# Kernel tuning notes

Measured on AMD Instinct MI355X. Metric: run time of the kernel, lower is better.

The kernel has to match this reference:

```python
import jax, jax.numpy as jnp
import numpy as np

ALPHA = 0.5
EPS = 1e-10

def setup_inputs() -> dict:
    key = jax.random.key(0)
    k1, k2, k3, k4 = jax.random.split(key, 4)
    B, S, H = 8, 2048, 768
    query_embs = jax.random.normal(k1, (B, S, H), dtype=jnp.float32)
    key_embs = jax.random.normal(k2, (B, S, H), dtype=jnp.float32)
    q_mask = (jax.random.uniform(k3, (B, S)) > 0.1).astype(jnp.float32)
    k_mask = (jax.random.uniform(k4, (B, S)) > 0.1).astype(jnp.float32)
    q_mask = q_mask.at[:, 0].set(1.0)
    k_mask = k_mask.at[:, 0].set(1.0)
    return {"query_embs": query_embs, "key_embs": key_embs,
            "q_mask": q_mask, "k_mask": k_mask, "gumbel_temp": 1.0}

def _l2norm(x):
    # torch F.normalize: x / max(||x||, eps-ish); use rsqrt with tiny floor
    n = jnp.sqrt(jnp.sum(x * x, axis=-1, keepdims=True))
    return x / jnp.maximum(n, 1e-12)

def reference(query_embs, key_embs, q_mask, k_mask, gumbel_temp):
    B, S, H = query_embs.shape
    q = _l2norm(query_embs)
    k = _l2norm(key_embs)
    sim = jnp.einsum('bqh,bkh->bqk', q, k)  # [B,S,S]
    # exponential distance decay w_{ij} = exp(-alpha*|i-j|)
    pos = jnp.arange(S)
    dist = jnp.abs(pos[:, None] - pos[None, :]).astype(sim.dtype)
    sim = sim * jnp.exp(-ALPHA * dist)
    valid = q_mask[:, :, None] * k_mask[:, None, :]  # [B,S,S]
    # eval path: no Gumbel noise
    noisy = sim / gumbel_temp
    noisy = noisy * valid - (1.0 - valid) * 1e9
    p = jax.nn.softmax(noisy, axis=-1)
    agg = jnp.einsum('bqk,bkh->bqh', p, k)
    scores = jnp.sum(q * agg, axis=-1) * q_mask  # [B,S]
    denom = jnp.maximum(jnp.sum(q_mask, axis=-1), 1.0)
    return jnp.sum(scores, axis=-1) / denom  # [B]
```

## Files before the change

kernel.cpp:

```cpp
#include <hip/hip_runtime.h>
#include <math.h>

#define SB 8
#define SS 2048
#define SH 768
#define ALPHA 0.5f

typedef __fp16 f16x8 __attribute__((ext_vector_type(8)));
typedef float f32x4 __attribute__((ext_vector_type(4)));

__device__ __forceinline__ float dot4(float4 a, float4 b) {
  return a.x*b.x + a.y*b.y + a.z*b.z + a.w*b.w;
}
__device__ __forceinline__ unsigned int pk2(float a, float b) {
  return __builtin_bit_cast(unsigned int, __builtin_amdgcn_cvt_pkrtz(a, b));
}


__global__ __launch_bounds__(256) void kprep_kernel(
    const float* __restrict__ K, const float* __restrict__ km,
    const float* __restrict__ qm,
    __fp16* __restrict__ Khs, float* __restrict__ ksum,
    float* __restrict__ Nk, float* __restrict__ qsum) {
  __shared__ float4 red[4][3][64];
  int b = blockIdx.y, jc = blockIdx.x, t = threadIdx.x;
  int w = t >> 6, lane = t & 63;
  int j0 = jc * 32;
  float4 acc0 = {0,0,0,0}, acc1 = {0,0,0,0}, acc2 = {0,0,0,0};
  for (int jj = 0; jj < 8; ++jj) {
    int j = j0 + 8 * w + jj;
    const float4* rp = (const float4*)(K + ((size_t)b * SS + j) * SH);
    float4 a = rp[lane], b4 = rp[lane + 64], c4 = rp[lane + 128];
    float ssv = dot4(a, a) + dot4(b4, b4) + dot4(c4, c4);
    #pragma unroll
    for (int m = 1; m < 64; m <<= 1) ssv += __shfl_xor(ssv, m, 64);
    float kwj = km[b * SS + j] / fmaxf(sqrtf(ssv), 1e-12f);
    uint2* kr = (uint2*)(Khs + ((size_t)b * SS + j) * SH);
    kr[lane]       = make_uint2(pk2(a.x*kwj,  a.y*kwj),  pk2(a.z*kwj,  a.w*kwj));
    kr[lane + 64]  = make_uint2(pk2(b4.x*kwj, b4.y*kwj), pk2(b4.z*kwj, b4.w*kwj));
    kr[lane + 128] = make_uint2(pk2(c4.x*kwj, c4.y*kwj), pk2(c4.z*kwj, c4.w*kwj));
    acc0.x += a.x*kwj;  acc0.y += a.y*kwj;  acc0.z += a.z*kwj;  acc0.w += a.w*kwj;
    acc1.x += b4.x*kwj; acc1.y += b4.y*kwj; acc1.z += b4.z*kwj; acc1.w += b4.w*kwj;
    acc2.x += c4.x*kwj; acc2.y += c4.y*kwj; acc2.z += c4.z*kwj; acc2.w += c4.w*kwj;
  }
  red[w][0][lane] = acc0; red[w][1][lane] = acc1; red[w][2][lane] = acc2;
  __syncthreads();
  if (t < 192) {
    int s = t >> 6, l = t & 63;
    float4 r0 = red[0][s][l], r1 = red[1][s][l], r2 = red[2][s][l], r3 = red[3][s][l];
    float* kp = ksum + b * SH + (s * 64 + l) * 4;
    atomicAdd(kp + 0, r0.x+r1.x+r2.x+r3.x);
    atomicAdd(kp + 1, r0.y+r1.y+r2.y+r3.y);
    atomicAdd(kp + 2, r0.z+r1.z+r2.z+r3.z);
    atomicAdd(kp + 3, r0.w+r1.w+r2.w+r3.w);
  }
  if (t < 32) {
    float pkm = km[b * SS + j0 + t];
    float pqm = qm[b * SS + j0 + t];
    #pragma unroll
    for (int m = 1; m < 32; m <<= 1) {
      pkm += __shfl_xor(pkm, m, 64);
      pqm += __shfl_xor(pqm, m, 64);
    }
    if (t == 0) { atomicAdd(&Nk[b], pkm); atomicAdd(&qsum[b], pqm); }
  }
}

__global__ __launch_bounds__(256, 1) void band_kernel(
    const float* __restrict__ Q, const __fp16* __restrict__ Khs,
    const float* __restrict__ temp, const float* __restrict__ qm,
    const float* __restrict__ ksum, const float* __restrict__ Nkp,
    const float* __restrict__ qsum,
    float* __restrict__ acc, int* __restrict__ cnt, float* __restrict__ out) {
  __shared__ float tab_s[64];
  int tid = threadIdx.x;
  int w = tid >> 6, lane = tid & 63;
  int l15 = lane & 15, quad = lane >> 4;
  int blk = blockIdx.x;
  int work = (blk & 7) * 32 + (blk >> 3);
  int b = work >> 5;
  int i0 = (work & 31) * 64;
  int i0w = i0 + 16 * w;
  int qrow = i0w + l15;

  float qmv = qm[b * SS + qrow];
  float nk = Nkp[b];
  {
    float invt = 1.0f / temp[0];
    tab_s[lane] = __expf(-ALPHA * fabsf((float)(lane - 31))) * invt;
  }
  asm volatile("s_waitcnt lgkmcnt(0)" ::: "memory");

  const float* qp = Q + ((size_t)b * SS + qrow) * SH + quad * 8;
  const float* kp = ksum + (size_t)b * SH + quad * 8;
  f16x8 afr[24];
  float ss = 0.f, dd = 0.f;
  #pragma unroll
  for (int s = 0; s < 24; ++s) {
    float4 x0 = *(const float4*)(qp + 32 * s);
    float4 x1 = *(const float4*)(qp + 32 * s + 4);
    float4 k0 = *(const float4*)(kp + 32 * s);
    float4 k1 = *(const float4*)(kp + 32 * s + 4);
    ss += dot4(x0, x0) + dot4(x1, x1);
    dd += dot4(x0, k0) + dot4(x1, k1);
    uint4 u = make_uint4(pk2(x0.x, x0.y), pk2(x0.z, x0.w),
                         pk2(x1.x, x1.y), pk2(x1.z, x1.w));
    afr[s] = __builtin_bit_cast(f16x8, u);
  }
  ss += __shfl_xor(ss, 16, 64); ss += __shfl_xor(ss, 32, 64);
  dd += __shfl_xor(dd, 16, 64); dd += __shfl_xor(dd, 32, 64);
  float qw = qmv / fmaxf(sqrtf(ss), 1e-12f);
  float qwsr[4], d0r[4];
  #pragma unroll
  for (int r = 0; r < 4; ++r) {
    qwsr[r] = __shfl(qw, quad * 4 + r, 64);
    d0r[r]  = __shfl(dd, quad * 4 + r, 64);
  }

  const __fp16* KbH = Khs + (size_t)b * SS * SH;
  f16x8 bqA[12], bqB[12];
  {
    int j = i0w - 32 + l15;
    int jc = min(max(j, 0), SS - 1);
    const __fp16* rp = KbH + (size_t)jc * SH + quad * 8;
    #pragma unroll
    for (int u = 0; u < 12; ++u) bqA[u] = *(const f16x8*)(rp + u * 32);
  }
  float an[4] = {0,0,0,0}, ad[4] = {0,0,0,0};
  f32x4 da = {0,0,0,0}, db = {0,0,0,0};
  #pragma unroll
  for (int fi = 0; fi < 10; ++fi) {
    const int t = fi >> 1, g = fi & 1;
    if (fi < 9) {
      const int tn = (fi + 1) >> 1, gn = (fi + 1) & 1;
      int j = i0w - 32 + 16 * tn + l15;
      int jc = min(max(j, 0), SS - 1);
      const __fp16* rp = KbH + (size_t)jc * SH + gn * 384 + quad * 8;
      #pragma unroll
      for (int u = 0; u < 12; ++u) {
        f16x8 v = *(const f16x8*)(rp + u * 32);
        if (fi & 1) bqA[u] = v; else bqB[u] = v;
      }
    }
    #pragma unroll
    for (int u = 0; u < 12; ++u) {
      f16x8 bv = (fi & 1) ? bqB[u] : bqA[u];
      if (u & 1) db = __builtin_amdgcn_mfma_f32_16x16x32_f16(afr[g*12+u], bv, db, 0, 0, 0);
      else       da = __builtin_amdgcn_mfma_f32_16x16x32_f16(afr[g*12+u], bv, da, 0, 0, 0);
    }
    if (g) {
      f32x4 ds = da + db;
      int j = i0w - 32 + 16 * t + l15;
      float vmask = ((unsigned)j < SS) ? 1.0f : 0.0f;
      int idxb = j - i0w + 31;
      #pragma unroll
      for (int reg = 0; reg < 4; ++reg) {
        float sv = ds[reg] * qwsr[reg];
        int idx = min(max(idxb - quad * 4 - reg, 0), 63);
        float ev = (__expf(sv * tab_s[idx]) - 1.0f) * vmask;
        an[reg] += ev * sv;
        ad[reg] += ev;
      }
      da = (f32x4){0,0,0,0}; db = (f32x4){0,0,0,0};
    }
  }

  float tot = 0.f;
  #pragma unroll
  for (int reg = 0; reg < 4; ++reg) {
    float a = an[reg], e = ad[reg];
    a += __shfl_xor(a, 1, 64); a += __shfl_xor(a, 2, 64);
    a += __shfl_xor(a, 4, 64); a += __shfl_xor(a, 8, 64);
    e += __shfl_xor(e, 1, 64); e += __shfl_xor(e, 2, 64);
    e += __shfl_xor(e, 4, 64); e += __shfl_xor(e, 8, 64);
    tot += (qwsr[reg] * d0r[reg] + a) / (nk + e);
  }
  tot += __shfl_xor(tot, 16, 64);
  tot += __shfl_xor(tot, 32, 64);
  if (lane == 0) {
    atomicAdd(&acc[b], tot);
    __threadfence();
    if (atomicAdd(&cnt[b], 1) == 127) {
      float a2 = atomicAdd(&acc[b], 0.0f);
      out[b] = a2 / fmaxf(qsum[b], 1.0f);
    }
  }
}

extern "C" void kernel_launch(void* const* d_in, const int* in_sizes, int n_in,
                              void* d_out, int out_size, void* d_ws, size_t ws_size,
                              hipStream_t stream) {
  const float* Q    = (const float*)d_in[0];
  const float* K    = (const float*)d_in[1];
  const float* qm   = (const float*)d_in[2];
  const float* km   = (const float*)d_in[3];
  const float* temp = (const float*)d_in[4];
  float* outp = (float*)d_out;

  const size_t KHS_BYTES = (size_t)SB * SS * SH * 2;
  __fp16* Khs = (__fp16*)d_ws;
  float* ksum = (float*)((char*)d_ws + KHS_BYTES);
  float* Nk   = ksum + SB * SH;
  float* qsum = Nk + 8;
  float* accb = qsum + 8;
  int*   cnt  = (int*)(accb + 8);

  (void)hipMemsetAsync(ksum, 0, (SB * SH + 32) * sizeof(float), stream);

  kprep_kernel<<<dim3(64, SB), 256, 0, stream>>>(K, km, qm, Khs, ksum, Nk, qsum);
  band_kernel<<<SB * (SS / 64), 256, 0, stream>>>(Q, Khs, temp, qm, ksum, Nk,
                                                  qsum, accb, cnt, outp);
}
```

Measured before the change: 179.2 us.

## Split band key tiles across wave pairs with explicit asm load pipelining

Each group of 16 query rows is now handled by two waves: one covers key tiles 0-2, the other tiles 3-4. Blocks cover 32 rows instead of 64, the grid doubles to 512 blocks, and launch bounds allow two blocks per CU. This aims to raise occupancy and cut each wave's serial chain of key loads and MFMAs. Key-tile loads are issued with inline global_load asm and explicit vmcnt waits, so loads overlap the MFMAs. Partial sums are combined through LDS before the per-batch atomic. The cost is that both waves of a pair load and normalise the same query rows, and the tile split between the two waves is uneven (three tiles against two).

```diff
diff --git a/kernel.cpp b/kernel.cpp
--- a/kernel.cpp
+++ b/kernel.cpp
@@ -14,6 +14,31 @@
 }
 __device__ __forceinline__ unsigned int pk2(float a, float b) {
   return __builtin_bit_cast(unsigned int, __builtin_amdgcn_cvt_pkrtz(a, b));
+}
+
+#define GLOAD(d, p, imm) \
+  asm volatile("global_load_dwordx4 %0, %1, off offset:" #imm \
+               : "=v"(d) : "v"(p) : "memory")
+#define ISSUE_LO(B, P) do { \
+  GLOAD(B[0],P,0);    GLOAD(B[1],P,64);   GLOAD(B[2],P,128);  \
+  GLOAD(B[3],P,192);  GLOAD(B[4],P,256);  GLOAD(B[5],P,320);  \
+  GLOAD(B[6],P,384);  GLOAD(B[7],P,448);  GLOAD(B[8],P,512);  \
+  GLOAD(B[9],P,576);  GLOAD(B[10],P,640); GLOAD(B[11],P,704); } while (0)
+#define ISSUE_HI(B, P) do { \
+  GLOAD(B[0],P,768);  GLOAD(B[1],P,832);  GLOAD(B[2],P,896);  \
+  GLOAD(B[3],P,960);  GLOAD(B[4],P,1024); GLOAD(B[5],P,1088); \
+  GLOAD(B[6],P,1152); GLOAD(B[7],P,1216); GLOAD(B[8],P,1280); \
+  GLOAD(B[9],P,1344); GLOAD(B[10],P,1408); GLOAD(B[11],P,1472); } while (0)
+#define WAITV(n) asm volatile("s_waitcnt vmcnt(" #n ")" ::: "memory")
+#define SB0() __builtin_amdgcn_sched_barrier(0)
+
+__device__ __forceinline__ void mfma12(const f16x8* a, const f16x8* B,
+                                       f32x4& da, f32x4& db) {
+  #pragma unroll
+  for (int u = 0; u < 12; ++u) {
+    if (u & 1) db = __builtin_amdgcn_mfma_f32_16x16x32_f16(a[u], B[u], db, 0, 0, 0);
+    else       da = __builtin_amdgcn_mfma_f32_16x16x32_f16(a[u], B[u], da, 0, 0, 0);
+  }
 }
 
 
@@ -66,22 +91,26 @@
   }
 }
 
-__global__ __launch_bounds__(256, 1) void band_kernel(
+__global__ __launch_bounds__(256, 2) void band_kernel(
     const float* __restrict__ Q, const __fp16* __restrict__ Khs,
     const float* __restrict__ temp, const float* __restrict__ qm,
     const float* __restrict__ ksum, const float* __restrict__ Nkp,
     const float* __restrict__ qsum,
     float* __restrict__ acc, int* __restrict__ cnt, float* __restrict__ out) {
   __shared__ float tab_s[64];
+  __shared__ float anS[2][2][16], adS[2][2][16];
+  __shared__ float qwS[2][16], d0S[2][16];
   int tid = threadIdx.x;
   int w = tid >> 6, lane = tid & 63;
   int l15 = lane & 15, quad = lane >> 4;
+  int rg = w >> 1, h = w & 1;
   int blk = blockIdx.x;
-  int work = (blk & 7) * 32 + (blk >> 3);
-  int b = work >> 5;
-  int i0 = (work & 31) * 64;
-  int i0w = i0 + 16 * w;
+  int work = (blk & 7) * 64 + (blk >> 3);
+  int b = work >> 6;
+  int i0 = (work & 63) * 32;
+  int i0w = i0 + 16 * rg;
   int qrow = i0w + l15;
+  int jbase = i0w - 32;
 
   float qmv = qm[b * SS + qrow];
   float nk = Nkp[b];
@@ -118,54 +147,55 @@
   }
 
   const __fp16* KbH = Khs + (size_t)b * SS * SH;
-  f16x8 bqA[12], bqB[12];
-  {
-    int j = i0w - 32 + l15;
-    int jc = min(max(j, 0), SS - 1);
-    const __fp16* rp = KbH + (size_t)jc * SH + quad * 8;
-    #pragma unroll
-    for (int u = 0; u < 12; ++u) bqA[u] = *(const f16x8*)(rp + u * 32);
-  }
+  auto tp = [&](int t) {
+    int jc = min(max(jbase + 16 * t + l15, 0), SS - 1);
+    return KbH + (size_t)jc * SH + quad * 8;
+  };
+
   float an[4] = {0,0,0,0}, ad[4] = {0,0,0,0};
   f32x4 da = {0,0,0,0}, db = {0,0,0,0};
-  #pragma unroll
-  for (int fi = 0; fi < 10; ++fi) {
-    const int t = fi >> 1, g = fi & 1;
-    if (fi < 9) {
-      const int tn = (fi + 1) >> 1, gn = (fi + 1) & 1;
-      int j = i0w - 32 + 16 * tn + l15;
-      int jc = min(max(j, 0), SS - 1);
-      const __fp16* rp = KbH + (size_t)jc * SH + gn * 384 + quad * 8;
-      #pragma unroll
-      for (int u = 0; u < 12; ++u) {
-        f16x8 v = *(const f16x8*)(rp + u * 32);
-        if (fi & 1) bqA[u] = v; else bqB[u] = v;
-      }
+  auto epi = [&](int t) {
+    f32x4 ds = da + db;
+    int j = jbase + 16 * t + l15;
+    float vmask = ((unsigned)j < SS) ? 1.0f : 0.0f;
+    int idxb = 16 * t + l15 - 1;
+    #pragma unroll
+    for (int reg = 0; reg < 4; ++reg) {
+      float sv = ds[reg] * qwsr[reg];
+      int idx = min(max(idxb - quad * 4 - reg, 0), 63);
+      float ev = (__expf(sv * tab_s[idx]) - 1.0f) * vmask;
+      an[reg] += ev * sv;
+      ad[reg] += ev;
     }
-    #pragma unroll
-    for (int u = 0; u < 12; ++u) {
-      f16x8 bv = (fi & 1) ? bqB[u] : bqA[u];
-      if (u & 1) db = __builtin_amdgcn_mfma_f32_16x16x32_f16(afr[g*12+u], bv, db, 0, 0, 0);
-      else       da = __builtin_amdgcn_mfma_f32_16x16x32_f16(afr[g*12+u], bv, da, 0, 0, 0);
-    }
-    if (g) {
-      f32x4 ds = da + db;
-      int j = i0w - 32 + 16 * t + l15;
-      float vmask = ((unsigned)j < SS) ? 1.0f : 0.0f;
-      int idxb = j - i0w + 31;
-      #pragma unroll
-      for (int reg = 0; reg < 4; ++reg) {
-        float sv = ds[reg] * qwsr[reg];
-        int idx = min(max(idxb - quad * 4 - reg, 0), 63);
-        float ev = (__expf(sv * tab_s[idx]) - 1.0f) * vmask;
-        an[reg] += ev * sv;
-        ad[reg] += ev;
-      }
-      da = (f32x4){0,0,0,0}; db = (f32x4){0,0,0,0};
-    }
-  }
-
-  float tot = 0.f;
+    da = (f32x4){0,0,0,0}; db = (f32x4){0,0,0,0};
+  };
+
+  f16x8 bqA[12], bqB[12];
+  WAITV(0);
+  if (h == 0) {
+    const __fp16* P0 = tp(0); const __fp16* P1 = tp(1); const __fp16* P2 = tp(2);
+    ISSUE_LO(bqA, P0); ISSUE_HI(bqB, P0);
+    WAITV(12); SB0(); mfma12(afr,      bqA, da, db);
+    ISSUE_LO(bqA, P1);
+    WAITV(12); SB0(); mfma12(afr + 12, bqB, da, db); epi(0);
+    ISSUE_HI(bqB, P1);
+    WAITV(12); SB0(); mfma12(afr,      bqA, da, db);
+    ISSUE_LO(bqA, P2);
+    WAITV(12); SB0(); mfma12(afr + 12, bqB, da, db); epi(1);
+    ISSUE_HI(bqB, P2);
+    WAITV(12); SB0(); mfma12(afr,      bqA, da, db);
+    WAITV(0);  SB0(); mfma12(afr + 12, bqB, da, db); epi(2);
+  } else {
+    const __fp16* P3 = tp(3); const __fp16* P4 = tp(4);
+    ISSUE_LO(bqA, P3); ISSUE_HI(bqB, P3);
+    WAITV(12); SB0(); mfma12(afr,      bqA, da, db);
+    ISSUE_LO(bqA, P4);
+    WAITV(12); SB0(); mfma12(afr + 12, bqB, da, db); epi(3);
+    ISSUE_HI(bqB, P4);
+    WAITV(12); SB0(); mfma12(afr,      bqA, da, db);
+    WAITV(0);  SB0(); mfma12(afr + 12, bqB, da, db); epi(4);
+  }
+
   #pragma unroll
   for (int reg = 0; reg < 4; ++reg) {
     float a = an[reg], e = ad[reg];
@@ -173,16 +203,25 @@
     a += __shfl_xor(a, 4, 64); a += __shfl_xor(a, 8, 64);
     e += __shfl_xor(e, 1, 64); e += __shfl_xor(e, 2, 64);
     e += __shfl_xor(e, 4, 64); e += __shfl_xor(e, 8, 64);
-    tot += (qwsr[reg] * d0r[reg] + a) / (nk + e);
-  }
-  tot += __shfl_xor(tot, 16, 64);
-  tot += __shfl_xor(tot, 32, 64);
-  if (lane == 0) {
-    atomicAdd(&acc[b], tot);
-    __threadfence();
-    if (atomicAdd(&cnt[b], 1) == 127) {
-      float a2 = atomicAdd(&acc[b], 0.0f);
-      out[b] = a2 / fmaxf(qsum[b], 1.0f);
+    if (l15 == 0) { anS[rg][h][quad * 4 + reg] = a; adS[rg][h][quad * 4 + reg] = e; }
+  }
+  if (h == 0 && lane < 16) { qwS[rg][lane] = qw; d0S[rg][lane] = dd; }
+  __syncthreads();
+  if (tid < 32) {
+    int rgc = tid >> 4, rr = tid & 15;
+    float a = anS[rgc][0][rr] + anS[rgc][1][rr];
+    float e = adS[rgc][0][rr] + adS[rgc][1][rr];
+    float sc = (qwS[rgc][rr] * d0S[rgc][rr] + a) / (nk + e);
+    sc += __shfl_xor(sc, 1, 64); sc += __shfl_xor(sc, 2, 64);
+    sc += __shfl_xor(sc, 4, 64); sc += __shfl_xor(sc, 8, 64);
+    sc += __shfl_xor(sc, 16, 64);
+    if (tid == 0) {
+      atomicAdd(&acc[b], sc);
+      __threadfence();
+      if (atomicAdd(&cnt[b], 1) == 63) {
+        float a2 = atomicAdd(&acc[b], 0.0f);
+        out[b] = a2 / fmaxf(qsum[b], 1.0f);
+      }
     }
   }
 }
@@ -208,6 +247,6 @@
   (void)hipMemsetAsync(ksum, 0, (SB * SH + 32) * sizeof(float), stream);
 
   kprep_kernel<<<dim3(64, SB), 256, 0, stream>>>(K, km, qm, Khs, ksum, Nk, qsum);
-  band_kernel<<<SB * (SS / 64), 256, 0, stream>>>(Q, Khs, temp, qm, ksum, Nk,
-                                                  qsum, accb, cnt, outp);
-}
+  band_kernel<<<512, 256, 0, stream>>>(Q, Khs, temp, qm, ksum, Nk,
+                                       qsum, accb, cnt, outp);
+}
```

After: 169.6 us. -5.4%, faster.

## Split hidden dim across waves and raise block count in both kernels

Applied to the files above, without the earlier changes.

The band kernel now gives each block 16 query rows instead of 64. Its four waves each take a 192-wide slice of the hidden dimension, and the partial MFMA tiles plus the norm and dot sums are combined through shared memory before the exp/softmax step. Loads for Q and for the fp16 K tiles are issued with inline global_load_dwordx4, double-buffered and bounded by explicit vmcnt waits, and launch bounds allow 4 blocks per CU. kprep is also re-gridded to 1024 blocks of 16 rows, so both kernels expose more parallel work to hide memory latency. In exchange the kernel pays for an LDS reduction, a __syncthreads, and redundant epilogue work across waves.

```diff
diff --git a/kernel.cpp b/kernel.cpp
--- a/kernel.cpp
+++ b/kernel.cpp
@@ -15,6 +15,15 @@
 __device__ __forceinline__ unsigned int pk2(float a, float b) {
   return __builtin_bit_cast(unsigned int, __builtin_amdgcn_cvt_pkrtz(a, b));
 }
+
+#define GLD(d, p, imm) \
+  asm volatile("global_load_dwordx4 %0, %1, off offset:" #imm \
+               : "=v"(d) : "v"(p) : "memory")
+#define WAITV(n) asm volatile("s_waitcnt vmcnt(" #n ")" ::: "memory")
+#define SB0() __builtin_amdgcn_sched_barrier(0)
+#define ISSUE_B(B, P) do { \
+  GLD(B[0],P,0);   GLD(B[1],P,64);  GLD(B[2],P,128); \
+  GLD(B[3],P,192); GLD(B[4],P,256); GLD(B[5],P,320); } while (0)
 
 
 __global__ __launch_bounds__(256) void kprep_kernel(
@@ -23,12 +32,14 @@
     __fp16* __restrict__ Khs, float* __restrict__ ksum,
     float* __restrict__ Nk, float* __restrict__ qsum) {
   __shared__ float4 red[4][3][64];
-  int b = blockIdx.y, jc = blockIdx.x, t = threadIdx.x;
+  int blk = blockIdx.x, t = threadIdx.x;
   int w = t >> 6, lane = t & 63;
-  int j0 = jc * 32;
+  int work = (blk & 7) * 128 + (blk >> 3);
+  int b = work >> 7;
+  int j0 = (work & 127) * 16;
   float4 acc0 = {0,0,0,0}, acc1 = {0,0,0,0}, acc2 = {0,0,0,0};
-  for (int jj = 0; jj < 8; ++jj) {
-    int j = j0 + 8 * w + jj;
+  for (int jj = 0; jj < 4; ++jj) {
+    int j = j0 + 4 * w + jj;
     const float4* rp = (const float4*)(K + ((size_t)b * SS + j) * SH);
     float4 a = rp[lane], b4 = rp[lane + 64], c4 = rp[lane + 128];
     float ssv = dot4(a, a) + dot4(b4, b4) + dot4(c4, c4);
@@ -54,11 +65,11 @@
     atomicAdd(kp + 2, r0.z+r1.z+r2.z+r3.z);
     atomicAdd(kp + 3, r0.w+r1.w+r2.w+r3.w);
   }
-  if (t < 32) {
+  if (t < 16) {
     float pkm = km[b * SS + j0 + t];
     float pqm = qm[b * SS + j0 + t];
     #pragma unroll
-    for (int m = 1; m < 32; m <<= 1) {
+    for (int m = 1; m < 16; m <<= 1) {
       pkm += __shfl_xor(pkm, m, 64);
       pqm += __shfl_xor(pqm, m, 64);
     }
@@ -66,105 +77,111 @@
   }
 }
 
-__global__ __launch_bounds__(256, 1) void band_kernel(
+__global__ __launch_bounds__(256, 4) void band_kernel(
     const float* __restrict__ Q, const __fp16* __restrict__ Khs,
     const float* __restrict__ temp, const float* __restrict__ qm,
     const float* __restrict__ ksum, const float* __restrict__ Nkp,
     const float* __restrict__ qsum,
     float* __restrict__ acc, int* __restrict__ cnt, float* __restrict__ out) {
+  __shared__ f32x4 sP[4][5][64];
+  __shared__ float sSS[4][16], sDD[4][16];
   __shared__ float tab_s[64];
   int tid = threadIdx.x;
   int w = tid >> 6, lane = tid & 63;
   int l15 = lane & 15, quad = lane >> 4;
   int blk = blockIdx.x;
-  int work = (blk & 7) * 32 + (blk >> 3);
-  int b = work >> 5;
-  int i0 = (work & 31) * 64;
-  int i0w = i0 + 16 * w;
-  int qrow = i0w + l15;
-
-  float qmv = qm[b * SS + qrow];
+  int work = (blk & 7) * 128 + (blk >> 3);
+  int b = work >> 7;
+  int i0 = (work & 127) * 16;
+
+  if (tid < 64) {
+    float invt = 1.0f / temp[0];
+    tab_s[tid] = __expf(-ALPHA * fabsf((float)(tid - 31))) * invt;
+  }
   float nk = Nkp[b];
-  {
-    float invt = 1.0f / temp[0];
-    tab_s[lane] = __expf(-ALPHA * fabsf((float)(lane - 31))) * invt;
-  }
-  asm volatile("s_waitcnt lgkmcnt(0)" ::: "memory");
-
-  const float* qp = Q + ((size_t)b * SS + qrow) * SH + quad * 8;
-  const float* kp = ksum + (size_t)b * SH + quad * 8;
-  f16x8 afr[24];
+
+  const char* qpB = (const char*)(Q + ((size_t)b * SS + i0 + l15) * SH
+                                  + w * 192 + quad * 8);
+  const float* ksb = ksum + (size_t)b * SH + w * 192 + quad * 8;
+  float4 xq[12];
+  GLD(xq[0],qpB,0);    GLD(xq[1],qpB,16);   GLD(xq[2],qpB,128);
+  GLD(xq[3],qpB,144);  GLD(xq[4],qpB,256);  GLD(xq[5],qpB,272);
+  GLD(xq[6],qpB,384);  GLD(xq[7],qpB,400);  GLD(xq[8],qpB,512);
+  GLD(xq[9],qpB,528);  GLD(xq[10],qpB,640); GLD(xq[11],qpB,656);
+  float4 ks0[6], ks1[6];
+  #pragma unroll
+  for (int s = 0; s < 6; ++s) {
+    ks0[s] = *(const float4*)(ksb + 32 * s);
+    ks1[s] = *(const float4*)(ksb + 32 * s + 4);
+  }
+  WAITV(0); SB0();
+  f16x8 afr[6];
   float ss = 0.f, dd = 0.f;
   #pragma unroll
-  for (int s = 0; s < 24; ++s) {
-    float4 x0 = *(const float4*)(qp + 32 * s);
-    float4 x1 = *(const float4*)(qp + 32 * s + 4);
-    float4 k0 = *(const float4*)(kp + 32 * s);
-    float4 k1 = *(const float4*)(kp + 32 * s + 4);
+  for (int s = 0; s < 6; ++s) {
+    float4 x0 = xq[2*s], x1 = xq[2*s+1];
     ss += dot4(x0, x0) + dot4(x1, x1);
-    dd += dot4(x0, k0) + dot4(x1, k1);
+    dd += dot4(x0, ks0[s]) + dot4(x1, ks1[s]);
     uint4 u = make_uint4(pk2(x0.x, x0.y), pk2(x0.z, x0.w),
                          pk2(x1.x, x1.y), pk2(x1.z, x1.w));
     afr[s] = __builtin_bit_cast(f16x8, u);
   }
   ss += __shfl_xor(ss, 16, 64); ss += __shfl_xor(ss, 32, 64);
   dd += __shfl_xor(dd, 16, 64); dd += __shfl_xor(dd, 32, 64);
-  float qw = qmv / fmaxf(sqrtf(ss), 1e-12f);
-  float qwsr[4], d0r[4];
-  #pragma unroll
-  for (int r = 0; r < 4; ++r) {
-    qwsr[r] = __shfl(qw, quad * 4 + r, 64);
-    d0r[r]  = __shfl(dd, quad * 4 + r, 64);
-  }
+  if (quad == 0) { sSS[w][l15] = ss; sDD[w][l15] = dd; }
 
   const __fp16* KbH = Khs + (size_t)b * SS * SH;
-  f16x8 bqA[12], bqB[12];
-  {
-    int j = i0w - 32 + l15;
-    int jc = min(max(j, 0), SS - 1);
-    const __fp16* rp = KbH + (size_t)jc * SH + quad * 8;
+  const char* pt[5];
+  #pragma unroll
+  for (int t = 0; t < 5; ++t) {
+    int jc = min(max(i0 - 32 + 16 * t + l15, 0), SS - 1);
+    pt[t] = (const char*)(KbH + (size_t)jc * SH + w * 192 + quad * 8);
+  }
+  f16x8 bqA[6], bqB[6];
+  auto dotile = [&](f16x8* bq, int t) {
+    f32x4 da = {0,0,0,0}, db = {0,0,0,0};
+    da = __builtin_amdgcn_mfma_f32_16x16x32_f16(afr[0], bq[0], da, 0, 0, 0);
+    db = __builtin_amdgcn_mfma_f32_16x16x32_f16(afr[1], bq[1], db, 0, 0, 0);
+    da = __builtin_amdgcn_mfma_f32_16x16x32_f16(afr[2], bq[2], da, 0, 0, 0);
+    db = __builtin_amdgcn_mfma_f32_16x16x32_f16(afr[3], bq[3], db, 0, 0, 0);
+    da = __builtin_amdgcn_mfma_f32_16x16x32_f16(afr[4], bq[4], da, 0, 0, 0);
+    db = __builtin_amdgcn_mfma_f32_16x16x32_f16(afr[5], bq[5], db, 0, 0, 0);
+    sP[w][t][lane] = da + db;
+  };
+  ISSUE_B(bqA, pt[0]); ISSUE_B(bqB, pt[1]);
+  WAITV(6); SB0(); dotile(bqA, 0); ISSUE_B(bqA, pt[2]);
+  WAITV(6); SB0(); dotile(bqB, 1); ISSUE_B(bqB, pt[3]);
+  WAITV(6); SB0(); dotile(bqA, 2); ISSUE_B(bqA, pt[4]);
+  WAITV(6); SB0(); dotile(bqB, 3);
+  WAITV(0); SB0(); dotile(bqA, 4);
+
+  __syncthreads();
+
+  float qws[4], d0s[4];
+  #pragma unroll
+  for (int reg = 0; reg < 4; ++reg) {
+    int r = quad * 4 + reg;
+    float ssr = sSS[0][r] + sSS[1][r] + sSS[2][r] + sSS[3][r];
+    float ddr = sDD[0][r] + sDD[1][r] + sDD[2][r] + sDD[3][r];
+    qws[reg] = qm[b * SS + i0 + r] / fmaxf(sqrtf(ssr), 1e-12f);
+    d0s[reg] = ddr;
+  }
+  float an[4] = {0,0,0,0}, ad[4] = {0,0,0,0};
+  #pragma unroll
+  for (int t = 0; t < 5; ++t) {
+    f32x4 v = sP[0][t][lane] + sP[1][t][lane] + sP[2][t][lane] + sP[3][t][lane];
+    int j = i0 - 32 + 16 * t + l15;
+    float vmask = ((unsigned)j < SS) ? 1.0f : 0.0f;
+    int idxb = 16 * t + l15 - 1;
     #pragma unroll
-    for (int u = 0; u < 12; ++u) bqA[u] = *(const f16x8*)(rp + u * 32);
-  }
-  float an[4] = {0,0,0,0}, ad[4] = {0,0,0,0};
-  f32x4 da = {0,0,0,0}, db = {0,0,0,0};
-  #pragma unroll
-  for (int fi = 0; fi < 10; ++fi) {
-    const int t = fi >> 1, g = fi & 1;
-    if (fi < 9) {
-      const int tn = (fi + 1) >> 1, gn = (fi + 1) & 1;
-      int j = i0w - 32 + 16 * tn + l15;
-      int jc = min(max(j, 0), SS - 1);
-      const __fp16* rp = KbH + (size_t)jc * SH + gn * 384 + quad * 8;
-      #pragma unroll
-      for (int u = 0; u < 12; ++u) {
-        f16x8 v = *(const f16x8*)(rp + u * 32);
-        if (fi & 1) bqA[u] = v; else bqB[u] = v;
-      }
+    for (int reg = 0; reg < 4; ++reg) {
+      float sv = v[reg] * qws[reg];
+      int idx = min(max(idxb - quad * 4 - reg, 0), 63);
+      float ev = (__expf(sv * tab_s[idx]) - 1.0f) * vmask;
+      an[reg] += ev * sv;
+      ad[reg] += ev;
     }
-    #pragma unroll
-    for (int u = 0; u < 12; ++u) {
-      f16x8 bv = (fi & 1) ? bqB[u] : bqA[u];
-      if (u & 1) db = __builtin_amdgcn_mfma_f32_16x16x32_f16(afr[g*12+u], bv, db, 0, 0, 0);
-      else       da = __builtin_amdgcn_mfma_f32_16x16x32_f16(afr[g*12+u], bv, da, 0, 0, 0);
-    }
-    if (g) {
-      f32x4 ds = da + db;
-      int j = i0w - 32 + 16 * t + l15;
-      float vmask = ((unsigned)j < SS) ? 1.0f : 0.0f;
-      int idxb = j - i0w + 31;
-      #pragma unroll
-      for (int reg = 0; reg < 4; ++reg) {
-        float sv = ds[reg] * qwsr[reg];
-        int idx = min(max(idxb - quad * 4 - reg, 0), 63);
-        float ev = (__expf(sv * tab_s[idx]) - 1.0f) * vmask;
-        an[reg] += ev * sv;
-        ad[reg] += ev;
-      }
-      da = (f32x4){0,0,0,0}; db = (f32x4){0,0,0,0};
-    }
-  }
-
+  }
   float tot = 0.f;
   #pragma unroll
   for (int reg = 0; reg < 4; ++reg) {
@@ -173,11 +190,11 @@
     a += __shfl_xor(a, 4, 64); a += __shfl_xor(a, 8, 64);
     e += __shfl_xor(e, 1, 64); e += __shfl_xor(e, 2, 64);
     e += __shfl_xor(e, 4, 64); e += __shfl_xor(e, 8, 64);
-    tot += (qwsr[reg] * d0r[reg] + a) / (nk + e);
+    tot += (qws[reg] * d0s[reg] + a) / (nk + e);
   }
   tot += __shfl_xor(tot, 16, 64);
   tot += __shfl_xor(tot, 32, 64);
-  if (lane == 0) {
+  if (tid == 0) {
     atomicAdd(&acc[b], tot);
     __threadfence();
     if (atomicAdd(&cnt[b], 1) == 127) {
@@ -207,7 +224,7 @@
 
   (void)hipMemsetAsync(ksum, 0, (SB * SH + 32) * sizeof(float), stream);
 
-  kprep_kernel<<<dim3(64, SB), 256, 0, stream>>>(K, km, qm, Khs, ksum, Nk, qsum);
-  band_kernel<<<SB * (SS / 64), 256, 0, stream>>>(Q, Khs, temp, qm, ksum, Nk,
-                                                  qsum, accb, cnt, outp);
-}
+  kprep_kernel<<<1024, 256, 0, stream>>>(K, km, qm, Khs, ksum, Nk, qsum);
+  band_kernel<<<1024, 256, 0, stream>>>(Q, Khs, temp, qm, ksum, Nk,
+                                        qsum, accb, cnt, outp);
+}
```

New measurement: 198.4 us. 10.7% more time.
